# Performance work log

Hardware: AMD Instinct MI355X
Metric: run time of the kernel (lower is better)

## Reference

```python
import jax, jax.numpy as jnp
import numpy as np

N_ATOMS = 10000
N_EDGES = 250000
F_DIM = 128
N_RBF = 20
CUTOFF = 5.0
N_INT = 3
EPS = 1e-8


def setup_inputs() -> dict:
    key = jax.random.key(0)
    ks = jax.random.split(key, 16)
    inp = {}
    inp["atomic_numbers"] = jax.random.randint(ks[0], (N_ATOMS,), 1, 101)
    # positions in a 5 Angstrom box so many pairs lie inside the cutoff
    inp["R"] = jax.random.uniform(ks[1], (N_ATOMS, 3), dtype=jnp.float32) * 5.0
    idx_i = jnp.sort(jax.random.randint(ks[2], (N_EDGES,), 0, N_ATOMS))
    # ensure idx_j != idx_i so d_ij > 0
    idx_j = (idx_i + 1 + jax.random.randint(ks[3], (N_EDGES,), 0, N_ATOMS - 1)) % N_ATOMS
    inp["idx_i"] = idx_i
    inp["idx_j"] = idx_j
    inp["offsets"] = jnp.zeros((N_EDGES, 3), dtype=jnp.float32)

    def w(k, shape):
        fan_in = shape[-2]
        return jax.random.normal(k, shape, dtype=jnp.float32) / np.sqrt(fan_in).astype(np.float32)

    inp["emb"] = jax.random.normal(ks[4], (101, F_DIM), dtype=jnp.float32)
    inp["filt_W"] = w(ks[5], (N_RBF, 3 * F_DIM))
    inp["filt_b"] = jax.random.normal(ks[6], (3 * F_DIM,), dtype=jnp.float32) * 0.01
    inp["int_W1"] = w(ks[7], (N_INT, F_DIM, F_DIM))
    inp["int_b1"] = jnp.zeros((N_INT, 1, F_DIM), dtype=jnp.float32)
    inp["int_W2"] = w(ks[8], (N_INT, F_DIM, 3 * F_DIM))
    inp["int_b2"] = jnp.zeros((N_INT, 1, 3 * F_DIM), dtype=jnp.float32)
    inp["mix_Wmu"] = w(ks[9], (N_INT, F_DIM, 2 * F_DIM))
    inp["mix_W1"] = w(ks[10], (N_INT, 2 * F_DIM, F_DIM))
    inp["mix_b1"] = jnp.zeros((N_INT, 1, F_DIM), dtype=jnp.float32)
    inp["mix_W2"] = w(ks[11], (N_INT, F_DIM, 3 * F_DIM))
    inp["mix_b2"] = jnp.zeros((N_INT, 1, 3 * F_DIM), dtype=jnp.float32)
    return inp


def painn_forward(atomic_numbers, idx_i, idx_j, R, offsets, emb, filt_W, filt_b,
                  int_W1, int_b1, int_W2, int_b2,
                  mix_Wmu, mix_W1, mix_b1, mix_W2, mix_b2):
    n_atoms = atomic_numbers.shape[0]
    # geometry
    r_ij = R[idx_j] - R[idx_i] + offsets                      # [E,3]
    d_ij = jnp.linalg.norm(r_ij, axis=1, keepdims=True)       # [E,1]
    dir_ij = r_ij / d_ij                                      # [E,3]
    # Gaussian radial basis + cosine cutoff (schnetpack defaults)
    centers = jnp.linspace(0.0, CUTOFF, N_RBF, dtype=jnp.float32)
    coeff = -0.5 / (centers[1] - centers[0]) ** 2
    phi = jnp.exp(coeff * (d_ij[..., None] - centers) ** 2)   # [E,1,N_RBF]
    fcut = 0.5 * (jnp.cos(d_ij * (jnp.pi / CUTOFF)) + 1.0) * (d_ij < CUTOFF)  # [E,1]
    Wij = (phi @ filt_W + filt_b) * fcut[..., None]           # [E,1,3F] (shared filters)

    q = emb[atomic_numbers][:, None, :]                       # [N,1,F]
    mu = jnp.zeros((n_atoms, 3, F_DIM), dtype=q.dtype)        # [N,3,F]

    for i in range(N_INT):
        # ---- interaction (equivariant message passing) ----
        x = jax.nn.silu(q @ int_W1[i] + int_b1[i]) @ int_W2[i] + int_b2[i]  # [N,1,3F]
        xj = x[idx_j]                                          # [E,1,3F]
        muj = mu[idx_j]                                        # [E,3,F]
        xw = Wij * xj                                          # [E,1,3F]
        dq, dmuR, dmumu = jnp.split(xw, 3, axis=-1)            # each [E,1,F]
        dq = jax.ops.segment_sum(dq, idx_i, num_segments=n_atoms)          # [N,1,F]
        dmu = dmuR * dir_ij[..., None] + dmumu * muj           # [E,3,F]
        dmu = jax.ops.segment_sum(dmu, idx_i, num_segments=n_atoms)        # [N,3,F]
        q = q + dq
        mu = mu + dmu
        # ---- mixing (intra-atomic) ----
        mu_mix = mu @ mix_Wmu[i]                               # [N,3,2F]
        mu_V, mu_W = jnp.split(mu_mix, 2, axis=-1)             # [N,3,F] each
        mu_Vn = jnp.sqrt(jnp.sum(mu_V ** 2, axis=-2, keepdims=True) + EPS)  # [N,1,F]
        ctx = jnp.concatenate([q, mu_Vn], axis=-1)             # [N,1,2F]
        xm = jax.nn.silu(ctx @ mix_W1[i] + mix_b1[i]) @ mix_W2[i] + mix_b2[i]  # [N,1,3F]
        dq_intra, dmu_intra, dqmu_intra = jnp.split(xm, 3, axis=-1)
        dmu_intra = dmu_intra * mu_W                           # [N,3,F]
        dqmu_intra = dqmu_intra * jnp.sum(mu_V * mu_W, axis=1, keepdims=True)  # [N,1,F]
        q = q + dq_intra + dqmu_intra
        mu = mu + dmu_intra

    return q.squeeze(1), mu                                    # [N,F], [N,3,F]


def reference(atomic_numbers, R, idx_i, idx_j, offsets, emb, filt_W, filt_b,
              int_W1, int_b1, int_W2, int_b2,
              mix_Wmu, mix_W1, mix_b1, mix_W2, mix_b2):
    return painn_forward(atomic_numbers, idx_i, idx_j, R, offsets, emb, filt_W, filt_b,
                         int_W1, int_b1, int_W2, int_b2,
                         mix_Wmu, mix_W1, mix_b1, mix_W2, mix_b2)
```

## Files before the change

### kernel.cpp

```cpp
#include <hip/hip_runtime.h>
#include <math.h>

#define NA 10000
#define NE 250000
#define FD 128
#define NRBF 20
#define RCUT 5.0f

typedef _Float16 h16;
typedef __attribute__((ext_vector_type(8))) _Float16 half8;
typedef __attribute__((ext_vector_type(2))) _Float16 half2v;
typedef __attribute__((ext_vector_type(4))) float f32x4;

static __device__ __forceinline__ half8 f32x8_to_h8(const float* p) {
    float4 a = *(const float4*)p;
    float4 b = *(const float4*)(p + 4);
    half8 r;
    r[0] = (h16)a.x; r[1] = (h16)a.y; r[2] = (h16)a.z; r[3] = (h16)a.w;
    r[4] = (h16)b.x; r[5] = (h16)b.y; r[6] = (h16)b.z; r[7] = (h16)b.w;
    return r;
}
static __device__ __forceinline__ float silu(float v) {
    return v / (1.f + expf(-v));
}

__global__ __launch_bounds__(256) void setup_kernel(
    const float* __restrict__ R, const int* __restrict__ idx_i,
    const int* __restrict__ idx_j, const float* __restrict__ offsets,
    float* __restrict__ dir, h16* __restrict__ ph, int* __restrict__ row_start,
    const float* __restrict__ int_W1, const float* __restrict__ int_W2,
    const float* __restrict__ mix_Wmu, const float* __restrict__ mix_W1,
    const float* __restrict__ mix_W2,
    h16* __restrict__ W1t, h16* __restrict__ W2t, h16* __restrict__ WmuT,
    h16* __restrict__ mW1t, h16* __restrict__ mW2t,
    const float* __restrict__ filt_W, const float* __restrict__ filt_b,
    h16* __restrict__ fwt)
{
    const int b = blockIdx.x;
    if (b < 977) {
        int e = b * 256 + threadIdx.x;
        if (e >= NE) return;
        int i = idx_i[e], j = idx_j[e];
        float rx = R[j * 3 + 0] - R[i * 3 + 0] + offsets[e * 3 + 0];
        float ry = R[j * 3 + 1] - R[i * 3 + 1] + offsets[e * 3 + 1];
        float rz = R[j * 3 + 2] - R[i * 3 + 2] + offsets[e * 3 + 2];
        float d = sqrtf(rx * rx + ry * ry + rz * rz);
        float inv = 1.f / d;
        float fcut = 0.f;
        if (d < RCUT) fcut = 0.5f * (cosf(d * (3.14159265358979323846f / RCUT)) + 1.f);
        *(float4*)&dir[(size_t)e * 4] = make_float4(rx * inv, ry * inv, rz * inv, 0.f);
        h16* pp = ph + (size_t)e * 32;
        const float delta = RCUT / 19.f;
        const float coeff = -0.5f / (delta * delta);
#pragma unroll
        for (int r = 0; r < NRBF; ++r) {
            float dc = d - (float)r * delta;
            pp[r] = (h16)(expf(coeff * dc * dc) * fcut);
        }
        pp[20] = (h16)fcut;
#pragma unroll
        for (int r = 21; r < 32; ++r) pp[r] = (h16)0.f;
    } else if (b < 1017) {
        int n = (b - 977) * 256 + threadIdx.x;
        if (n > NA) return;
        int lo = 0, hi = NE;
        while (lo < hi) {
            int mid = (lo + hi) >> 1;
            if (idx_i[mid] < n) lo = mid + 1; else hi = mid;
        }
        row_start[n] = lo;
    } else {
        int idx = (b - 1017) * 256 + threadIdx.x;
        if (idx < 49152) {
            int bt = idx >> 14, rem = idx & 16383;
            int nn = rem >> 7, kk = rem & 127;
            W1t[idx] = (h16)int_W1[(size_t)bt * 16384 + kk * 128 + nn];
        } else if ((idx -= 49152) < 147456) {
            int bt = idx / 49152, rem = idx - bt * 49152;
            int nn = rem >> 7, kk = rem & 127;
            W2t[idx] = (h16)int_W2[(size_t)bt * 49152 + kk * 384 + nn];
        } else if ((idx -= 147456) < 98304) {
            int bt = idx >> 15, rem = idx & 32767;
            int nn = rem >> 7, kk = rem & 127;
            WmuT[idx] = (h16)mix_Wmu[(size_t)bt * 32768 + kk * 256 + nn];
        } else if ((idx -= 98304) < 98304) {
            int bt = idx >> 15, rem = idx & 32767;
            int nn = rem >> 8, kk = rem & 255;
            mW1t[idx] = (h16)mix_W1[(size_t)bt * 32768 + kk * 128 + nn];
        } else if ((idx -= 98304) < 147456) {
            int bt = idx / 49152, rem = idx - bt * 49152;
            int nn = rem >> 7, kk = rem & 127;
            mW2t[idx] = (h16)mix_W2[(size_t)bt * 49152 + kk * 384 + nn];
        } else if ((idx -= 147456) < 12288) {
            int nn = idx >> 5, kk = idx & 31;
            float v = 0.f;
            if (kk < 20) v = filt_W[kk * 384 + nn];
            else if (kk == 20) v = filt_b[nn];
            fwt[idx] = (h16)v;
        }
    }
}

__global__ __launch_bounds__(256) void intmlp0_kernel(
    const int* __restrict__ Z, const float* __restrict__ emb, float* __restrict__ q,
    const h16* __restrict__ W1t, const float* __restrict__ b1,
    const h16* __restrict__ W2t, const float* __restrict__ b2, h16* __restrict__ xm)
{
    __shared__ h16 Hs[16 * 136];
    const int tid = threadIdx.x;
    const int wave = tid >> 6, lane = tid & 63;
    const int ar = lane & 15, kg = lane >> 4;
    const size_t row0 = (size_t)blockIdx.x * 16;

    {
        int a = tid >> 4, f0 = (tid & 15) * 8;
        const float* src = emb + (size_t)Z[row0 + a] * 128 + f0;
        float4 v0 = *(const float4*)src;
        float4 v1 = *(const float4*)(src + 4);
        *(float4*)&q[(row0 + a) * 128 + f0] = v0;
        *(float4*)&q[(row0 + a) * 128 + f0 + 4] = v1;
    }
    const int zr = Z[row0 + ar];
    f32x4 a1[2] = {};
    for (int ks = 0; ks < 128; ks += 32) {
        int k = ks + kg * 8;
        half8 af = f32x8_to_h8(emb + (size_t)zr * 128 + k);
#pragma unroll
        for (int tt = 0; tt < 2; ++tt) {
            int t = wave * 2 + tt;
            half8 bf = *(const half8*)&W1t[(size_t)(t * 16 + ar) * 128 + k];
            a1[tt] = __builtin_amdgcn_mfma_f32_16x16x32_f16(af, bf, a1[tt], 0, 0, 0);
        }
    }
#pragma unroll
    for (int tt = 0; tt < 2; ++tt) {
        int col = (wave * 2 + tt) * 16 + ar;
        float bb = b1[col];
#pragma unroll
        for (int r = 0; r < 4; ++r)
            Hs[(kg * 4 + r) * 136 + col] = (h16)silu(a1[tt][r] + bb);
    }
    __syncthreads();
    f32x4 a2[6] = {};
    for (int ks = 0; ks < 128; ks += 32) {
        int k = ks + kg * 8;
        half8 af = *(const half8*)&Hs[ar * 136 + k];
#pragma unroll
        for (int tt = 0; tt < 6; ++tt) {
            int t = wave * 6 + tt;
            half8 bf = *(const half8*)&W2t[(size_t)(t * 16 + ar) * 128 + k];
            a2[tt] = __builtin_amdgcn_mfma_f32_16x16x32_f16(af, bf, a2[tt], 0, 0, 0);
        }
    }
#pragma unroll
    for (int tt = 0; tt < 6; ++tt) {
        int col = (wave * 6 + tt) * 16 + ar;
        float bb = b2[col];
        int slot = col >> 7, ff = col & 127;
#pragma unroll
        for (int r = 0; r < 4; ++r)
            xm[((size_t)(row0 + kg * 4 + r) * 128 + ff) * 6 + slot] = (h16)(a2[tt][r] + bb);
    }
}

template<bool HAS_MU>
__global__ __launch_bounds__(128, 5) void edge_kernel(
    const float* __restrict__ dir, const h16* __restrict__ ph,
    const h16* __restrict__ fwt,
    const int* __restrict__ row_start, const int* __restrict__ idx_j,
    const h16* __restrict__ xm, const float* __restrict__ mup,
    float* __restrict__ mun, h16* __restrict__ mu16n, float* __restrict__ q)
{
    const int n = blockIdx.x, f = threadIdx.x;
    half2v fa[12], fb[12], fc[12];
    {
        const half8* pa = (const half8*)(fwt + (size_t)f * 32);
        const half8* pb = (const half8*)(fwt + (size_t)(128 + f) * 32);
#pragma unroll
        for (int r = 0; r < 3; ++r) {
            *(half8*)&fa[r * 4] = pa[r];
            *(half8*)&fb[r * 4] = pb[r];
        }
        if (HAS_MU) {
            const half8* pc = (const half8*)(fwt + (size_t)(256 + f) * 32);
#pragma unroll
            for (int r = 0; r < 3; ++r)
                *(half8*)&fc[r * 4] = pc[r];
        }
    }
    const h16* xmf = xm + (size_t)f * 6;
    float accq = 0.f, am0 = 0.f, am1 = 0.f, am2 = 0.f;
    const int e0 = row_start[n], e1 = row_start[n + 1];
    for (int e = e0; e < e1; ++e) {
        int j = idx_j[e];
        const unsigned int* gp = (const unsigned int*)(xmf + (size_t)j * 768);
        unsigned int g0 = gp[0], g1 = gp[1], g2 = 0u;
        if (HAS_MU) g2 = gp[2];
        half2v pr[12];
        const h16* pb8 = ph + (size_t)e * 32;
        *(half8*)&pr[0] = *(const half8*)pb8;
        *(half8*)&pr[4] = *(const half8*)(pb8 + 8);
        *(half8*)&pr[8] = *(const half8*)(pb8 + 16);
        float4 g = *(const float4*)&dir[(size_t)e * 4];
        half2v A0 = {(h16)0.f, (h16)0.f}, A1 = A0, A2 = A0;
#pragma unroll
        for (int r = 0; r < 11; ++r) {
            A0 = pr[r] * fa[r] + A0;
            A1 = pr[r] * fb[r] + A1;
            if (HAS_MU) A2 = pr[r] * fc[r] + A2;
        }
        float w0 = (float)A0[0] + (float)A0[1];
        float w1 = (float)A1[0] + (float)A1[1];
        half2v h01 = __builtin_bit_cast(half2v, g0);
        half2v h23 = __builtin_bit_cast(half2v, g1);
        float x0 = (float)h01[0], x1 = (float)h01[1];
        accq = fmaf(w0, x0, accq);
        float xw1 = w1 * x1;
        if (HAS_MU) {
            float w2 = (float)A2[0] + (float)A2[1];
            half2v h45 = __builtin_bit_cast(half2v, g2);
            float x2 = (float)h23[0];
            float xw2 = w2 * x2;
            am0 += xw1 * g.x + xw2 * (float)h23[1];
            am1 += xw1 * g.y + xw2 * (float)h45[0];
            am2 += xw1 * g.z + xw2 * (float)h45[1];
        } else {
            am0 = fmaf(xw1, g.x, am0);
            am1 = fmaf(xw1, g.y, am1);
            am2 = fmaf(xw1, g.z, am2);
        }
    }
    q[(size_t)n * FD + f] += accq;
    size_t b = (size_t)n * 384;
    float m0 = (HAS_MU ? mup[b + f] : 0.f) + am0;
    float m1 = (HAS_MU ? mup[b + 128 + f] : 0.f) + am1;
    float m2 = (HAS_MU ? mup[b + 256 + f] : 0.f) + am2;
    mun[b + f] = m0; mun[b + 128 + f] = m1; mun[b + 256 + f] = m2;
    mu16n[b + f] = (h16)m0; mu16n[b + 128 + f] = (h16)m1; mu16n[b + 256 + f] = (h16)m2;
}

__global__ __launch_bounds__(256) void mixint_kernel(
    const h16* __restrict__ mu16n, const h16* __restrict__ WmuT,
    const h16* __restrict__ W1t, const float* __restrict__ b1,
    const h16* __restrict__ W2t, const float* __restrict__ b2,
    float* __restrict__ q, float* __restrict__ mu, h16* __restrict__ xmw,
    const h16* __restrict__ nW1t, const float* __restrict__ nb1,
    const h16* __restrict__ nW2t, const float* __restrict__ nb2)
{
    __shared__ h16 MM[48 * 264];
    __shared__ h16 CT[16 * 264];
    __shared__ h16 Hs[16 * 136];
    __shared__ h16 XM[16 * 392];
    const int tid = threadIdx.x;
    const int wave = tid >> 6, lane = tid & 63;
    const int ar = lane & 15, kg = lane >> 4;
    const size_t row0 = (size_t)blockIdx.x * 16;

    {
        f32x4 acc[3][4] = {};
        int aloc[3], dloc[3];
#pragma unroll
        for (int rt = 0; rt < 3; ++rt) {
            int rr = rt * 16 + ar;
            aloc[rt] = rr / 3;
            dloc[rt] = rr - 3 * aloc[rt];
        }
        for (int ks = 0; ks < 128; ks += 32) {
            int k = ks + kg * 8;
            half8 afr[3];
#pragma unroll
            for (int rt = 0; rt < 3; ++rt)
                afr[rt] = *(const half8*)&mu16n[(row0 + aloc[rt]) * 384 + dloc[rt] * 128 + k];
#pragma unroll
            for (int ct = 0; ct < 4; ++ct) {
                int cc = wave * 4 + ct;
                half8 bf = *(const half8*)&WmuT[(size_t)(cc * 16 + ar) * 128 + k];
#pragma unroll
                for (int rt = 0; rt < 3; ++rt)
                    acc[rt][ct] = __builtin_amdgcn_mfma_f32_16x16x32_f16(afr[rt], bf, acc[rt][ct], 0, 0, 0);
            }
        }
#pragma unroll
        for (int rt = 0; rt < 3; ++rt)
#pragma unroll
            for (int ct = 0; ct < 4; ++ct) {
                int col = (wave * 4 + ct) * 16 + ar;
#pragma unroll
                for (int r = 0; r < 4; ++r)
                    MM[(rt * 16 + kg * 4 + r) * 264 + col] = (h16)acc[rt][ct][r];
            }
    }
    __syncthreads();

    {
        int a = tid >> 4, fi = (tid & 15) * 8;
        const float* qp = q + (row0 + a) * 128 + fi;
        float4 q0 = *(const float4*)qp;
        float4 q1 = *(const float4*)(qp + 4);
        float qv[8] = {q0.x, q0.y, q0.z, q0.w, q1.x, q1.y, q1.z, q1.w};
#pragma unroll
        for (int jj = 0; jj < 8; ++jj) {
            int ff = fi + jj;
            float v0 = (float)MM[(a * 3 + 0) * 264 + ff];
            float v1 = (float)MM[(a * 3 + 1) * 264 + ff];
            float v2 = (float)MM[(a * 3 + 2) * 264 + ff];
            CT[a * 264 + 128 + ff] = (h16)sqrtf(v0 * v0 + v1 * v1 + v2 * v2 + 1e-8f);
            CT[a * 264 + ff] = (h16)qv[jj];
        }
    }
    __syncthreads();

    {
        f32x4 a1[2] = {};
        for (int ks = 0; ks < 256; ks += 32) {
            int k = ks + kg * 8;
            half8 af = *(const half8*)&CT[ar * 264 + k];
#pragma unroll
            for (int tt = 0; tt < 2; ++tt) {
                int t = wave * 2 + tt;
                half8 bf = *(const half8*)&W1t[(size_t)(t * 16 + ar) * 256 + k];
                a1[tt] = __builtin_amdgcn_mfma_f32_16x16x32_f16(af, bf, a1[tt], 0, 0, 0);
            }
        }
#pragma unroll
        for (int tt = 0; tt < 2; ++tt) {
            int col = (wave * 2 + tt) * 16 + ar;
            float bb = b1[col];
#pragma unroll
            for (int r = 0; r < 4; ++r)
                Hs[(kg * 4 + r) * 136 + col] = (h16)silu(a1[tt][r] + bb);
        }
    }
    __syncthreads();

    {
        f32x4 a2[6] = {};
        for (int ks = 0; ks < 128; ks += 32) {
            int k = ks + kg * 8;
            half8 af = *(const half8*)&Hs[ar * 136 + k];
#pragma unroll
            for (int tt = 0; tt < 6; ++tt) {
                int t = wave * 6 + tt;
                half8 bf = *(const half8*)&W2t[(size_t)(t * 16 + ar) * 128 + k];
                a2[tt] = __builtin_amdgcn_mfma_f32_16x16x32_f16(af, bf, a2[tt], 0, 0, 0);
            }
        }
#pragma unroll
        for (int tt = 0; tt < 6; ++tt) {
            int col = (wave * 6 + tt) * 16 + ar;
            float bb = b2[col];
#pragma unroll
            for (int r = 0; r < 4; ++r)
                XM[(kg * 4 + r) * 392 + col] = (h16)(a2[tt][r] + bb);
        }
    }
    __syncthreads();

    {
        int a = tid >> 4, fi = (tid & 15) * 8;
        size_t n = row0 + a;
#pragma unroll
        for (int jj = 0; jj < 8; ++jj) {
            int ff = fi + jj;
            float dq  = (float)XM[a * 392 + ff];
            float dm  = (float)XM[a * 392 + 128 + ff];
            float dqm = (float)XM[a * 392 + 256 + ff];
            float v0 = (float)MM[(a * 3 + 0) * 264 + ff], w0 = (float)MM[(a * 3 + 0) * 264 + 128 + ff];
            float v1 = (float)MM[(a * 3 + 1) * 264 + ff], w1 = (float)MM[(a * 3 + 1) * 264 + 128 + ff];
            float v2 = (float)MM[(a * 3 + 2) * 264 + ff], w2 = (float)MM[(a * 3 + 2) * 264 + 128 + ff];
            float sv = v0 * w0 + v1 * w1 + v2 * w2;
            float qn = q[n * 128 + ff] + dq + dqm * sv;
            q[n * 128 + ff] = qn;
            CT[a * 264 + ff] = (h16)qn;
            size_t b = n * 384 + ff;
            float m0 = mu[b] + dm * w0;
            float m1 = mu[b + 128] + dm * w1;
            float m2 = mu[b + 256] + dm * w2;
            mu[b] = m0; mu[b + 128] = m1; mu[b + 256] = m2;
            h16* xw = xmw + ((size_t)n * 128 + ff) * 6;
            xw[3] = (h16)m0; xw[4] = (h16)m1; xw[5] = (h16)m2;
        }
    }
    if (!nW1t) return;
    __syncthreads();

    {
        f32x4 a1[2] = {};
        for (int ks = 0; ks < 128; ks += 32) {
            int k = ks + kg * 8;
            half8 af = *(const half8*)&CT[ar * 264 + k];
#pragma unroll
            for (int tt = 0; tt < 2; ++tt) {
                int t = wave * 2 + tt;
                half8 bf = *(const half8*)&nW1t[(size_t)(t * 16 + ar) * 128 + k];
                a1[tt] = __builtin_amdgcn_mfma_f32_16x16x32_f16(af, bf, a1[tt], 0, 0, 0);
            }
        }
#pragma unroll
        for (int tt = 0; tt < 2; ++tt) {
            int col = (wave * 2 + tt) * 16 + ar;
            float bb = nb1[col];
#pragma unroll
            for (int r = 0; r < 4; ++r)
                Hs[(kg * 4 + r) * 136 + col] = (h16)silu(a1[tt][r] + bb);
        }
        __syncthreads();
        f32x4 a2[6] = {};
        for (int ks = 0; ks < 128; ks += 32) {
            int k = ks + kg * 8;
            half8 af = *(const half8*)&Hs[ar * 136 + k];
#pragma unroll
            for (int tt = 0; tt < 6; ++tt) {
                int t = wave * 6 + tt;
                half8 bf = *(const half8*)&nW2t[(size_t)(t * 16 + ar) * 128 + k];
                a2[tt] = __builtin_amdgcn_mfma_f32_16x16x32_f16(af, bf, a2[tt], 0, 0, 0);
            }
        }
#pragma unroll
        for (int tt = 0; tt < 6; ++tt) {
            int col = (wave * 6 + tt) * 16 + ar;
            float bb = nb2[col];
            int slot = col >> 7, ff = col & 127;
#pragma unroll
            for (int r = 0; r < 4; ++r)
                xmw[((size_t)(row0 + kg * 4 + r) * 128 + ff) * 6 + slot] = (h16)(a2[tt][r] + bb);
        }
    }
}

extern "C" void kernel_launch(void* const* d_in, const int* in_sizes, int n_in,
                              void* d_out, int out_size, void* d_ws, size_t ws_size,
                              hipStream_t stream)
{
    const int*   Z       = (const int*)d_in[0];
    const float* R       = (const float*)d_in[1];
    const int*   idx_i   = (const int*)d_in[2];
    const int*   idx_j   = (const int*)d_in[3];
    const float* offsets = (const float*)d_in[4];
    const float* emb     = (const float*)d_in[5];
    const float* filt_W  = (const float*)d_in[6];
    const float* filt_b  = (const float*)d_in[7];
    const float* int_W1  = (const float*)d_in[8];
    const float* int_b1  = (const float*)d_in[9];
    const float* int_W2  = (const float*)d_in[10];
    const float* int_b2  = (const float*)d_in[11];
    const float* mix_Wmu = (const float*)d_in[12];
    const float* mix_W1  = (const float*)d_in[13];
    const float* mix_b1  = (const float*)d_in[14];
    const float* mix_W2  = (const float*)d_in[15];
    const float* mix_b2  = (const float*)d_in[16];

    float* q_out  = (float*)d_out;
    float* mu_out = (float*)d_out + (size_t)NA * FD;

    char* base = (char*)d_ws;
    size_t o = 0;
    auto alloc = [&](size_t bytes) -> void* {
        void* p = base + o;
        o += (bytes + 255) & ~(size_t)255;
        return p;
    };
    float* dir    = (float*)alloc((size_t)NE * 4 * 4);
    h16*   ph     = (h16*)alloc((size_t)NE * 32 * 2);
    h16*   xm     = (h16*)alloc((size_t)NA * 128 * 6 * 2);
    h16*   mu16p  = (h16*)alloc((size_t)NA * 384 * 2);
    float* mu_ws  = (float*)alloc((size_t)NA * 384 * 4);
    h16*   W1t    = (h16*)alloc((size_t)3 * 128 * 128 * 2);
    h16*   W2t    = (h16*)alloc((size_t)3 * 384 * 128 * 2);
    h16*   WmuT   = (h16*)alloc((size_t)3 * 256 * 128 * 2);
    h16*   mW1t   = (h16*)alloc((size_t)3 * 128 * 256 * 2);
    h16*   mW2t   = (h16*)alloc((size_t)3 * 384 * 128 * 2);
    h16*   fwt    = (h16*)alloc((size_t)384 * 32 * 2);
    int*   row_st = (int*)alloc((size_t)(NA + 1) * 4);

    setup_kernel<<<3177, 256, 0, stream>>>(R, idx_i, idx_j, offsets, dir, ph, row_st,
                                           int_W1, int_W2, mix_Wmu, mix_W1, mix_W2,
                                           W1t, W2t, WmuT, mW1t, mW2t,
                                           filt_W, filt_b, fwt);

    intmlp0_kernel<<<NA / 16, 256, 0, stream>>>(Z, emb, q_out,
                                                W1t, int_b1, W2t, int_b2, xm);
    edge_kernel<false><<<NA, 128, 0, stream>>>(dir, ph, fwt, row_st, idx_j,
                                               xm, nullptr, mu_out, mu16p, q_out);
    mixint_kernel<<<NA / 16, 256, 0, stream>>>(
        mu16p, WmuT, mW1t, mix_b1, mW2t, mix_b2, q_out, mu_out, xm,
        W1t + 16384, int_b1 + 128, W2t + 49152, int_b2 + 384);

    edge_kernel<true><<<NA, 128, 0, stream>>>(dir, ph, fwt, row_st, idx_j,
                                              xm, mu_out, mu_ws, mu16p, q_out);
    mixint_kernel<<<NA / 16, 256, 0, stream>>>(
        mu16p, WmuT + 32768, mW1t + 32768, mix_b1 + 128, mW2t + 49152, mix_b2 + 384,
        q_out, mu_ws, xm,
        W1t + 32768, int_b1 + 256, W2t + 98304, int_b2 + 768);

    edge_kernel<true><<<NA, 128, 0, stream>>>(dir, ph, fwt, row_st, idx_j,
                                              xm, mu_ws, mu_out, mu16p, q_out);
    mixint_kernel<<<NA / 16, 256, 0, stream>>>(
        mu16p, WmuT + 65536, mW1t + 65536, mix_b1 + 256, mW2t + 98304, mix_b2 + 768,
        q_out, mu_out, xm,
        nullptr, nullptr, nullptr, nullptr);
}
```

Before: 493.7 us.

## Stage xm outputs in shared memory, prefetch next edge in edge kernel

The MLP kernels now write their interleaved fp16 xm tiles into shared memory and then copy them out with coalesced 16-byte stores, replacing scattered 2-byte global writes. The mixint kernel merges the mu halves into the same staged tile. The edge kernel software-pipelines its loop, loading the next edge's gather, basis and direction data while computing the current edge, and lowers the occupancy hint from 5 to 4 to make room for the extra registers. The added shared memory and registers may reduce occupancy. When the next-layer MLP is skipped, the mixint kernel returns early and the mu part of xmw is no longer written.

```diff
diff --git a/kernel.cpp b/kernel.cpp
--- a/kernel.cpp
+++ b/kernel.cpp
@@ -107,6 +107,7 @@
     const h16* __restrict__ W2t, const float* __restrict__ b2, h16* __restrict__ xm)
 {
     __shared__ h16 Hs[16 * 136];
+    __shared__ __align__(16) h16 XMP[16 * 128 * 6];
     const int tid = threadIdx.x;
     const int wave = tid >> 6, lane = tid & 63;
     const int ar = lane & 15, kg = lane >> 4;
@@ -159,12 +160,20 @@
         int slot = col >> 7, ff = col & 127;
 #pragma unroll
         for (int r = 0; r < 4; ++r)
-            xm[((size_t)(row0 + kg * 4 + r) * 128 + ff) * 6 + slot] = (h16)(a2[tt][r] + bb);
+            XMP[((kg * 4 + r) * 128 + ff) * 6 + slot] = (h16)(a2[tt][r] + bb);
+    }
+    __syncthreads();
+    {
+        const uint4* src = (const uint4*)XMP;
+        uint4* dst = (uint4*)(xm + row0 * 768);
+#pragma unroll
+        for (int i = 0; i < 6; ++i)
+            dst[tid + i * 256] = src[tid + i * 256];
     }
 }
 
 template<bool HAS_MU>
-__global__ __launch_bounds__(128, 5) void edge_kernel(
+__global__ __launch_bounds__(128, 4) void edge_kernel(
     const float* __restrict__ dir, const h16* __restrict__ ph,
     const h16* __restrict__ fwt,
     const int* __restrict__ row_start, const int* __restrict__ idx_j,
@@ -172,62 +181,88 @@
     float* __restrict__ mun, h16* __restrict__ mu16n, float* __restrict__ q)
 {
     const int n = blockIdx.x, f = threadIdx.x;
-    half2v fa[12], fb[12], fc[12];
+    half8 FA[3], FB[3], FC[3];
     {
         const half8* pa = (const half8*)(fwt + (size_t)f * 32);
         const half8* pb = (const half8*)(fwt + (size_t)(128 + f) * 32);
 #pragma unroll
-        for (int r = 0; r < 3; ++r) {
-            *(half8*)&fa[r * 4] = pa[r];
-            *(half8*)&fb[r * 4] = pb[r];
-        }
+        for (int r = 0; r < 3; ++r) { FA[r] = pa[r]; FB[r] = pb[r]; }
         if (HAS_MU) {
             const half8* pc = (const half8*)(fwt + (size_t)(256 + f) * 32);
 #pragma unroll
-            for (int r = 0; r < 3; ++r)
-                *(half8*)&fc[r * 4] = pc[r];
-        }
-    }
+            for (int r = 0; r < 3; ++r) FC[r] = pc[r];
+        }
+    }
+    asm volatile("" : "+v"(FA[0]), "+v"(FA[1]), "+v"(FA[2]),
+                      "+v"(FB[0]), "+v"(FB[1]), "+v"(FB[2]));
+    if (HAS_MU)
+        asm volatile("" : "+v"(FC[0]), "+v"(FC[1]), "+v"(FC[2]));
+
+    half2v fa[12], fb[12], fc[12];
+    *(half8*)&fa[0] = FA[0]; *(half8*)&fa[4] = FA[1]; *(half8*)&fa[8] = FA[2];
+    *(half8*)&fb[0] = FB[0]; *(half8*)&fb[4] = FB[1]; *(half8*)&fb[8] = FB[2];
+    if (HAS_MU) {
+        *(half8*)&fc[0] = FC[0]; *(half8*)&fc[4] = FC[1]; *(half8*)&fc[8] = FC[2];
+    }
+
     const h16* xmf = xm + (size_t)f * 6;
     float accq = 0.f, am0 = 0.f, am1 = 0.f, am2 = 0.f;
     const int e0 = row_start[n], e1 = row_start[n + 1];
-    for (int e = e0; e < e1; ++e) {
-        int j = idx_j[e];
-        const unsigned int* gp = (const unsigned int*)(xmf + (size_t)j * 768);
-        unsigned int g0 = gp[0], g1 = gp[1], g2 = 0u;
-        if (HAS_MU) g2 = gp[2];
-        half2v pr[12];
-        const h16* pb8 = ph + (size_t)e * 32;
-        *(half8*)&pr[0] = *(const half8*)pb8;
-        *(half8*)&pr[4] = *(const half8*)(pb8 + 8);
-        *(half8*)&pr[8] = *(const half8*)(pb8 + 16);
-        float4 g = *(const float4*)&dir[(size_t)e * 4];
-        half2v A0 = {(h16)0.f, (h16)0.f}, A1 = A0, A2 = A0;
-#pragma unroll
-        for (int r = 0; r < 11; ++r) {
-            A0 = pr[r] * fa[r] + A0;
-            A1 = pr[r] * fb[r] + A1;
-            if (HAS_MU) A2 = pr[r] * fc[r] + A2;
-        }
-        float w0 = (float)A0[0] + (float)A0[1];
-        float w1 = (float)A1[0] + (float)A1[1];
-        half2v h01 = __builtin_bit_cast(half2v, g0);
-        half2v h23 = __builtin_bit_cast(half2v, g1);
-        float x0 = (float)h01[0], x1 = (float)h01[1];
-        accq = fmaf(w0, x0, accq);
-        float xw1 = w1 * x1;
-        if (HAS_MU) {
-            float w2 = (float)A2[0] + (float)A2[1];
-            half2v h45 = __builtin_bit_cast(half2v, g2);
-            float x2 = (float)h23[0];
-            float xw2 = w2 * x2;
-            am0 += xw1 * g.x + xw2 * (float)h23[1];
-            am1 += xw1 * g.y + xw2 * (float)h45[0];
-            am2 += xw1 * g.z + xw2 * (float)h45[1];
-        } else {
-            am0 = fmaf(xw1, g.x, am0);
-            am1 = fmaf(xw1, g.y, am1);
-            am2 = fmaf(xw1, g.z, am2);
+    if (e0 < e1) {
+        int j = idx_j[e0];
+        const unsigned* gp = (const unsigned*)(xmf + (size_t)j * 768);
+        unsigned g0n = gp[0], g1n = gp[1], g2n = 0u;
+        if (HAS_MU) g2n = gp[2];
+        const h16* pb8 = ph + (size_t)e0 * 32;
+        half8 p0n = *(const half8*)pb8;
+        half8 p1n = *(const half8*)(pb8 + 8);
+        half8 p2n = *(const half8*)(pb8 + 16);
+        float4 dn = *(const float4*)&dir[(size_t)e0 * 4];
+        for (int e = e0; e < e1; ++e) {
+            unsigned g0 = g0n, g1 = g1n, g2 = g2n;
+            half8 p0 = p0n, p1 = p1n, p2 = p2n;
+            float4 g = dn;
+            int ep = (e + 1 < e1) ? e + 1 : e;
+            int j2 = idx_j[ep];
+            const unsigned* gp2 = (const unsigned*)(xmf + (size_t)j2 * 768);
+            g0n = gp2[0]; g1n = gp2[1];
+            if (HAS_MU) g2n = gp2[2];
+            const h16* pb2 = ph + (size_t)ep * 32;
+            p0n = *(const half8*)pb2;
+            p1n = *(const half8*)(pb2 + 8);
+            p2n = *(const half8*)(pb2 + 16);
+            dn = *(const float4*)&dir[(size_t)ep * 4];
+            half2v pr[12];
+            *(half8*)&pr[0] = p0; *(half8*)&pr[4] = p1; *(half8*)&pr[8] = p2;
+            half2v A0 = {(h16)0.f, (h16)0.f}, A1 = A0, A2 = A0;
+#pragma unroll
+            for (int r = 0; r < 11; ++r) {
+                A0 = pr[r] * fa[r] + A0;
+                A1 = pr[r] * fb[r] + A1;
+                if (HAS_MU) A2 = pr[r] * fc[r] + A2;
+            }
+            float w0 = (float)A0[0] + (float)A0[1];
+            float w1 = (float)A1[0] + (float)A1[1];
+            half2v h01 = __builtin_bit_cast(half2v, g0);
+            half2v h23 = __builtin_bit_cast(half2v, g1);
+            float x0 = (float)h01[0], x1 = (float)h01[1];
+            accq = fmaf(w0, x0, accq);
+            float xw1 = w1 * x1;
+            if (HAS_MU) {
+                float w2 = (float)A2[0] + (float)A2[1];
+                half2v h45 = __builtin_bit_cast(half2v, g2);
+                float x2 = (float)h23[0];
+                float xw2 = w2 * x2;
+                am0 += xw1 * g.x + xw2 * (float)h23[1];
+                am1 += xw1 * g.y + xw2 * (float)h45[0];
+                am2 += xw1 * g.z + xw2 * (float)h45[1];
+            } else {
+                float x2 = (float)h23[0];
+                (void)x2;
+                am0 = fmaf(xw1, g.x, am0);
+                am1 = fmaf(xw1, g.y, am1);
+                am2 = fmaf(xw1, g.z, am2);
+            }
         }
     }
     q[(size_t)n * FD + f] += accq;
@@ -247,7 +282,7 @@
     const h16* __restrict__ nW1t, const float* __restrict__ nb1,
     const h16* __restrict__ nW2t, const float* __restrict__ nb2)
 {
-    __shared__ h16 MM[48 * 264];
+    __shared__ __align__(16) h16 MM[48 * 264];
     __shared__ h16 CT[16 * 264];
     __shared__ h16 Hs[16 * 136];
     __shared__ h16 XM[16 * 392];
@@ -356,6 +391,7 @@
     }
     __syncthreads();
 
+    h16 mh[24];
     {
         int a = tid >> 4, fi = (tid & 15) * 8;
         size_t n = row0 + a;
@@ -377,8 +413,7 @@
             float m1 = mu[b + 128] + dm * w1;
             float m2 = mu[b + 256] + dm * w2;
             mu[b] = m0; mu[b + 128] = m1; mu[b + 256] = m2;
-            h16* xw = xmw + ((size_t)n * 128 + ff) * 6;
-            xw[3] = (h16)m0; xw[4] = (h16)m1; xw[5] = (h16)m2;
+            mh[jj * 3 + 0] = (h16)m0; mh[jj * 3 + 1] = (h16)m1; mh[jj * 3 + 2] = (h16)m2;
         }
     }
     if (!nW1t) return;
@@ -416,6 +451,7 @@
                 a2[tt] = __builtin_amdgcn_mfma_f32_16x16x32_f16(af, bf, a2[tt], 0, 0, 0);
             }
         }
+        h16* XMP = MM;
 #pragma unroll
         for (int tt = 0; tt < 6; ++tt) {
             int col = (wave * 6 + tt) * 16 + ar;
@@ -423,7 +459,23 @@
             int slot = col >> 7, ff = col & 127;
 #pragma unroll
             for (int r = 0; r < 4; ++r)
-                xmw[((size_t)(row0 + kg * 4 + r) * 128 + ff) * 6 + slot] = (h16)(a2[tt][r] + bb);
+                XMP[((kg * 4 + r) * 128 + ff) * 6 + slot] = (h16)(a2[tt][r] + bb);
+        }
+        {
+            int a = tid >> 4, fi = (tid & 15) * 8;
+#pragma unroll
+            for (int jj = 0; jj < 8; ++jj)
+#pragma unroll
+                for (int s = 0; s < 3; ++s)
+                    XMP[(a * 128 + fi + jj) * 6 + 3 + s] = mh[jj * 3 + s];
+        }
+        __syncthreads();
+        {
+            const uint4* src = (const uint4*)MM;
+            uint4* dst = (uint4*)(xmw + row0 * 768);
+#pragma unroll
+            for (int i = 0; i < 6; ++i)
+                dst[tid + i * 256] = src[tid + i * 256];
         }
     }
 }
```

Result: faster. 440.2 us (-10.8%).
